# Kernel optimization log

Measured on AMD Instinct MI355X. Metric: run time of the kernel, lower is better.

Reference implementation:

```python
import jax, jax.numpy as jnp
import numpy as np

KERNEL_SIZE = 7
CHANNELS = 3

def _box_filter(x):
    # Depthwise uniform box filter, 'same' padding (pad = k//2, k odd).
    k = KERNEL_SIZE
    kernel = jnp.full((CHANNELS, 1, k, k), 1.0 / (k * k), dtype=x.dtype)
    return jax.lax.conv_general_dilated(
        x, kernel,
        window_strides=(1, 1),
        padding=[(k // 2, k // 2), (k // 2, k // 2)],
        dimension_numbers=('NCHW', 'OIHW', 'NCHW'),
        feature_group_count=CHANNELS)

def setup_inputs() -> dict:
    key = jax.random.key(0)
    k1, k2 = jax.random.split(key)
    shape = (32, 3, 512, 512)
    pred = jax.random.normal(k1, shape, dtype=jnp.float32)
    target = jax.random.normal(k2, shape, dtype=jnp.float32)
    return {"pred": pred, "target": target}

def reference(pred, target):
    pred_contrast = pred - _box_filter(pred)
    target_contrast = target - _box_filter(target)
    return jnp.mean(jnp.abs(pred_contrast - target_contrast))
```

## Files before the change

### kernel.cpp

```cpp
#include <hip/hip_runtime.h>

namespace {
constexpr int H = 512;
constexpr int W = 512;
constexpr int NC = 96;
constexpr int RSTRIP = 32;
constexpr int NSTRIP = H / RSTRIP;
constexpr int NBLK = NC * NSTRIP;
constexpr int NTHR = 256;
constexpr float INV_K2 = 1.0f / 49.0f;
constexpr float INV_TOTAL = 1.0f / (32.0f * 3.0f * 512.0f * 512.0f);
}

__global__ __launch_bounds__(NTHR, 4) void lcl_partial(
    const float* __restrict__ pred, const float* __restrict__ target,
    float* __restrict__ partials)
{
    __shared__ __align__(16) float row_s[W + 8];
    __shared__ float wred[NTHR / 64];

    const int tid   = threadIdx.x;
    const int img   = blockIdx.x / NSTRIP;
    const int strip = blockIdx.x - img * NSTRIP;
    const int y0    = strip * RSTRIP;
    const int c0    = tid * 2;
    const size_t base = (size_t)img * (size_t)(H * W);

    if (tid < 4) { row_s[tid] = 0.0f; row_s[W + 4 + tid] = 0.0f; }

    float2 hring[7];
    float2 dring[4];
#pragma unroll
    for (int i = 0; i < 7; ++i) hring[i] = make_float2(0.f, 0.f);
#pragma unroll
    for (int i = 0; i < 4; ++i) dring[i] = make_float2(0.f, 0.f);

    float acc = 0.0f;

    for (int y = y0 - 3; y < y0 + RSTRIP + 3; ++y) {
        float2 v = make_float2(0.f, 0.f);
        if ((unsigned)y < (unsigned)H) {
            const size_t roff = base + (size_t)y * W + c0;
            const float2 a = *(const float2*)(pred + roff);
            const float2 b = *(const float2*)(target + roff);
            v.x = a.x - b.x;
            v.y = a.y - b.y;
        }
        __syncthreads();
        *(float2*)&row_s[4 + c0] = v;
        __syncthreads();

        const float w0 = row_s[c0 + 1];
        const float w1 = row_s[c0 + 2];
        const float w2 = row_s[c0 + 3];
        const float w3 = row_s[c0 + 4];
        const float w4 = row_s[c0 + 5];
        const float w5 = row_s[c0 + 6];
        const float w6 = row_s[c0 + 7];
        const float w7 = row_s[c0 + 8];
        const float hx = ((w0 + w1) + (w2 + w3)) + ((w4 + w5) + w6);
        const float hy = ((w1 + w2) + (w3 + w4)) + ((w5 + w6) + w7);

#pragma unroll
        for (int i = 6; i > 0; --i) hring[i] = hring[i - 1];
        hring[0] = make_float2(hx, hy);
#pragma unroll
        for (int i = 3; i > 0; --i) dring[i] = dring[i - 1];
        dring[0] = v;

        if (y >= y0 + 3) {
            const float vsx = ((hring[0].x + hring[1].x) + (hring[2].x + hring[3].x))
                            + ((hring[4].x + hring[5].x) + hring[6].x);
            const float vsy = ((hring[0].y + hring[1].y) + (hring[2].y + hring[3].y))
                            + ((hring[4].y + hring[5].y) + hring[6].y);
            const float ox = dring[3].x - vsx * INV_K2;
            const float oy = dring[3].y - vsy * INV_K2;
            acc += fabsf(ox) + fabsf(oy);
        }
    }

#pragma unroll
    for (int off = 32; off > 0; off >>= 1)
        acc += __shfl_down(acc, off, 64);
    if ((tid & 63) == 0) wred[tid >> 6] = acc;
    __syncthreads();
    if (tid == 0)
        partials[blockIdx.x] = (wred[0] + wred[1]) + (wred[2] + wred[3]);
}

__global__ __launch_bounds__(256) void lcl_reduce(const float* __restrict__ partials,
                                                  float* __restrict__ out)
{
    __shared__ float wred[4];
    const int tid = threadIdx.x;
    float s = 0.0f;
    for (int i = tid; i < NBLK; i += 256) s += partials[i];
#pragma unroll
    for (int off = 32; off > 0; off >>= 1)
        s += __shfl_down(s, off, 64);
    if ((tid & 63) == 0) wred[tid >> 6] = s;
    __syncthreads();
    if (tid == 0) out[0] = ((wred[0] + wred[1]) + (wred[2] + wred[3])) * INV_TOTAL;
}

extern "C" void kernel_launch(void* const* d_in, const int* in_sizes, int n_in,
                              void* d_out, int out_size, void* d_ws, size_t ws_size,
                              hipStream_t stream) {
    const float* pred   = (const float*)d_in[0];
    const float* target = (const float*)d_in[1];
    float* out      = (float*)d_out;
    float* partials = (float*)d_ws;

    lcl_partial<<<NBLK, NTHR, 0, stream>>>(pred, target, partials);
    lcl_reduce<<<1, 256, 0, stream>>>(partials, out);
}
```

Baseline: 41.53 us.

## Stage full strip tile in LDS and use running vertical box sum

Each block now loads its whole 38-row strip (32 rows plus halo) into shared memory with float4 loads in one bulk phase and a single barrier. Previously it loaded row by row with two barriers per row. Threads now own one column each (512 threads), and the vertical 7-tap sum becomes a sliding running sum over compile-time-indexed ring registers. The aim is to cut synchronisation and redundant adds and to widen memory accesses. In exchange it uses about 79 KB of LDS per block, which limits occupancy, and all loads are serialized ahead of compute.

After: 47.69 us. +14.8%, slower.

```diff
diff --git a/kernel.cpp b/kernel.cpp
--- a/kernel.cpp
+++ b/kernel.cpp
@@ -5,87 +5,116 @@
 constexpr int W = 512;
 constexpr int NC = 96;
 constexpr int RSTRIP = 32;
-constexpr int NSTRIP = H / RSTRIP;
-constexpr int NBLK = NC * NSTRIP;
-constexpr int NTHR = 256;
+constexpr int SPP = H / RSTRIP;
+constexpr int NBLK = NC * SPP;
+constexpr int NTHR = 512;
+constexpr int TROWS = RSTRIP + 6;
+constexpr int LROW = W + 8;
+constexpr int NF4 = TROWS * (W / 4);
 constexpr float INV_K2 = 1.0f / 49.0f;
 constexpr float INV_TOTAL = 1.0f / (32.0f * 3.0f * 512.0f * 512.0f);
 }
 
+template <int P8, int P4, bool EMIT>
+__device__ __forceinline__ void step(const float* __restrict__ lds_row,
+                                     float (&hr)[8], float (&dr)[4],
+                                     float& vs, float& acc)
+{
+    const float w0 = lds_row[0];
+    const float w1 = lds_row[1];
+    const float w2 = lds_row[2];
+    const float w3 = lds_row[3];
+    const float w4 = lds_row[4];
+    const float w5 = lds_row[5];
+    const float w6 = lds_row[6];
+    const float h = ((w0 + w1) + (w2 + w3)) + ((w4 + w5) + w6);
+
+    constexpr int S  = P8 & 7;
+    constexpr int So = (P8 + 1) & 7;
+    constexpr int Q  = P4 & 3;
+    constexpr int Qo = (P4 + 1) & 3;
+
+    vs += h - hr[So];
+    hr[S] = h;
+    if (EMIT) acc += fabsf(dr[Qo] - vs * INV_K2);
+    dr[Q] = w3;
+}
+
 __global__ __launch_bounds__(NTHR, 4) void lcl_partial(
-    const float* __restrict__ pred, const float* __restrict__ target,
+    const float4* __restrict__ pred4, const float4* __restrict__ targ4,
     float* __restrict__ partials)
 {
-    __shared__ __align__(16) float row_s[W + 8];
-    __shared__ float wred[NTHR / 64];
+    __shared__ float sm[TROWS * LROW + 8];
 
-    const int tid   = threadIdx.x;
-    const int img   = blockIdx.x / NSTRIP;
-    const int strip = blockIdx.x - img * NSTRIP;
-    const int y0    = strip * RSTRIP;
-    const int c0    = tid * 2;
-    const size_t base = (size_t)img * (size_t)(H * W);
+    const int t     = threadIdx.x;
+    const int plane = blockIdx.x >> 4;
+    const int y0    = (blockIdx.x & 15) * RSTRIP;
+    const int base4 = plane * (H * (W / 4));
 
-    if (tid < 4) { row_s[tid] = 0.0f; row_s[W + 4 + tid] = 0.0f; }
-
-    float2 hring[7];
-    float2 dring[4];
-#pragma unroll
-    for (int i = 0; i < 7; ++i) hring[i] = make_float2(0.f, 0.f);
-#pragma unroll
-    for (int i = 0; i < 4; ++i) dring[i] = make_float2(0.f, 0.f);
-
-    float acc = 0.0f;
-
-    for (int y = y0 - 3; y < y0 + RSTRIP + 3; ++y) {
-        float2 v = make_float2(0.f, 0.f);
-        if ((unsigned)y < (unsigned)H) {
-            const size_t roff = base + (size_t)y * W + c0;
-            const float2 a = *(const float2*)(pred + roff);
-            const float2 b = *(const float2*)(target + roff);
-            v.x = a.x - b.x;
-            v.y = a.y - b.y;
-        }
-        __syncthreads();
-        *(float2*)&row_s[4 + c0] = v;
-        __syncthreads();
-
-        const float w0 = row_s[c0 + 1];
-        const float w1 = row_s[c0 + 2];
-        const float w2 = row_s[c0 + 3];
-        const float w3 = row_s[c0 + 4];
-        const float w4 = row_s[c0 + 5];
-        const float w5 = row_s[c0 + 6];
-        const float w6 = row_s[c0 + 7];
-        const float w7 = row_s[c0 + 8];
-        const float hx = ((w0 + w1) + (w2 + w3)) + ((w4 + w5) + w6);
-        const float hy = ((w1 + w2) + (w3 + w4)) + ((w5 + w6) + w7);
+    if (t < TROWS * 6) {
+        const int r = t / 6;
+        const int k = t - 6 * r;
+        sm[r * LROW + (k < 3 ? 1 + k : 513 + k)] = 0.f;
+    }
 
 #pragma unroll
-        for (int i = 6; i > 0; --i) hring[i] = hring[i - 1];
-        hring[0] = make_float2(hx, hy);
+    for (int it = 0; it < 10; ++it) {
+        const int i = t + it * NTHR;
+        if (it < 9 || i < NF4) {
+            const int r  = i >> 7;
+            const int cw = i & 127;
+            const int y  = y0 - 3 + r;
+            float4 d4 = make_float4(0.f, 0.f, 0.f, 0.f);
+            if ((unsigned)y < (unsigned)H) {
+                const float4 a = pred4[base4 + y * (W / 4) + cw];
+                const float4 b = targ4[base4 + y * (W / 4) + cw];
+                d4 = make_float4(a.x - b.x, a.y - b.y, a.z - b.z, a.w - b.w);
+            }
+            *(float4*)&sm[r * LROW + 4 + 4 * cw] = d4;
+        }
+    }
+    __syncthreads();
+
+    float hr[8], dr[4];
 #pragma unroll
-        for (int i = 3; i > 0; --i) dring[i] = dring[i - 1];
-        dring[0] = v;
+    for (int s = 0; s < 8; ++s) hr[s] = 0.f;
+#pragma unroll
+    for (int s = 0; s < 4; ++s) dr[s] = 0.f;
+    float vs = 0.f, acc = 0.f;
 
-        if (y >= y0 + 3) {
-            const float vsx = ((hring[0].x + hring[1].x) + (hring[2].x + hring[3].x))
-                            + ((hring[4].x + hring[5].x) + hring[6].x);
-            const float vsy = ((hring[0].y + hring[1].y) + (hring[2].y + hring[3].y))
-                            + ((hring[4].y + hring[5].y) + hring[6].y);
-            const float ox = dring[3].x - vsx * INV_K2;
-            const float oy = dring[3].y - vsy * INV_K2;
-            acc += fabsf(ox) + fabsf(oy);
-        }
+    const float* p = &sm[t + 1];
+
+    step<0, 0, false>(p + 0 * LROW, hr, dr, vs, acc);
+    step<1, 1, false>(p + 1 * LROW, hr, dr, vs, acc);
+    step<2, 2, false>(p + 2 * LROW, hr, dr, vs, acc);
+    step<3, 3, false>(p + 3 * LROW, hr, dr, vs, acc);
+    step<4, 0, false>(p + 4 * LROW, hr, dr, vs, acc);
+    step<5, 1, false>(p + 5 * LROW, hr, dr, vs, acc);
+
+#pragma unroll 1
+    for (int b = 0; b < 4; ++b) {
+        const float* q = p + (6 + 8 * b) * LROW;
+        step<6, 2, true>(q + 0 * LROW, hr, dr, vs, acc);
+        step<7, 3, true>(q + 1 * LROW, hr, dr, vs, acc);
+        step<0, 0, true>(q + 2 * LROW, hr, dr, vs, acc);
+        step<1, 1, true>(q + 3 * LROW, hr, dr, vs, acc);
+        step<2, 2, true>(q + 4 * LROW, hr, dr, vs, acc);
+        step<3, 3, true>(q + 5 * LROW, hr, dr, vs, acc);
+        step<4, 0, true>(q + 6 * LROW, hr, dr, vs, acc);
+        step<5, 1, true>(q + 7 * LROW, hr, dr, vs, acc);
     }
 
 #pragma unroll
     for (int off = 32; off > 0; off >>= 1)
         acc += __shfl_down(acc, off, 64);
-    if ((tid & 63) == 0) wred[tid >> 6] = acc;
+    float* wred = &sm[TROWS * LROW];
+    if ((t & 63) == 0) wred[t >> 6] = acc;
     __syncthreads();
-    if (tid == 0)
-        partials[blockIdx.x] = (wred[0] + wred[1]) + (wred[2] + wred[3]);
+    if (t == 0) {
+        float s = ((wred[0] + wred[1]) + (wred[2] + wred[3]))
+                + ((wred[4] + wred[5]) + (wred[6] + wred[7]));
+        partials[blockIdx.x] = s;
+    }
 }
 
 __global__ __launch_bounds__(256) void lcl_reduce(const float* __restrict__ partials,
@@ -106,11 +135,11 @@
 extern "C" void kernel_launch(void* const* d_in, const int* in_sizes, int n_in,
                               void* d_out, int out_size, void* d_ws, size_t ws_size,
                               hipStream_t stream) {
-    const float* pred   = (const float*)d_in[0];
-    const float* target = (const float*)d_in[1];
+    const float4* pred4 = (const float4*)d_in[0];
+    const float4* targ4 = (const float4*)d_in[1];
     float* out      = (float*)d_out;
     float* partials = (float*)d_ws;
 
-    lcl_partial<<<NBLK, NTHR, 0, stream>>>(pred, target, partials);
+    lcl_partial<<<NBLK, NTHR, 0, stream>>>(pred4, targ4, partials);
     lcl_reduce<<<1, 256, 0, stream>>>(partials, out);
 }
```
